# Performance work log

Measured on AMD Instinct MI355X. Metric: run time of the kernel, lower is better.

The kernel has to match this reference:

```python
import jax, jax.numpy as jnp
import numpy as np

D_MODEL = 256; N_LAYERS = 4; INPUT_LEN = 15
D_INNER = 512; D_STATE = 16; D_CONV = 4; DT_RANK = 16
BATCH = 4; SEQ = 2048; EPS = 1e-5

def _ln(x, w, b):
    m = jnp.mean(x, -1, keepdims=True)
    v = jnp.var(x, -1, keepdims=True)
    return (x - m) * jax.lax.rsqrt(v + EPS) * w + b

def _silu(x):
    return x * jax.nn.sigmoid(x)

def _mixer(h, inW, cw, cb, xpW, dtW, dtb, A_log, Dp, opW):
    # h: [B,L,d_model]
    xz = h @ inW.T                      # [B,L,2*D_INNER]
    xh, z = jnp.split(xz, 2, axis=-1)
    # causal depthwise conv1d
    xc = jnp.transpose(xh, (0, 2, 1))   # [B,D,L]
    xc = jax.lax.conv_general_dilated(xc, cw, (1,), [(D_CONV - 1, 0)],
                                      feature_group_count=D_INNER,
                                      dimension_numbers=('NCH', 'OIH', 'NCH'))
    xc = xc + cb[None, :, None]
    xh = _silu(jnp.transpose(xc, (0, 2, 1)))  # [B,L,D]
    dbl = xh @ xpW.T                    # [B,L,DT_RANK+2N]
    dt = dbl[..., :DT_RANK]
    Bm = dbl[..., DT_RANK:DT_RANK + D_STATE]
    C = dbl[..., DT_RANK + D_STATE:]
    dt = jax.nn.softplus(dt @ dtW.T + dtb)    # [B,L,D]
    A = -jnp.exp(A_log)                       # [D,N]
    dA = jnp.exp(dt[..., None] * A)           # [B,L,D,N]
    dBu = dt[..., None] * Bm[:, :, None, :] * xh[..., None]  # [B,L,D,N]
    def step(hst, inp):
        dA_t, dBu_t, C_t = inp
        hst = dA_t * hst + dBu_t
        y = jnp.einsum('bdn,bn->bd', hst, C_t)
        return hst, y
    h0 = jnp.zeros((xh.shape[0], D_INNER, D_STATE), xh.dtype)
    _, ys = jax.lax.scan(step, h0, (jnp.transpose(dA, (1, 0, 2, 3)),
                                    jnp.transpose(dBu, (1, 0, 2, 3)),
                                    jnp.transpose(C, (1, 0, 2))))
    y = jnp.transpose(ys, (1, 0, 2)) + Dp * xh
    y = y * _silu(z)
    return y @ opW.T

def setup_inputs():
    key = jax.random.key(0)
    ks = jax.random.split(key, 8)
    s = 0.02
    return {
        'x_src': jax.random.normal(ks[0], (BATCH, SEQ, INPUT_LEN), jnp.float32),
        'single_eval_pos': 1024,
        'in_W': jax.random.normal(ks[1], (D_MODEL, INPUT_LEN)) * s,
        'norm_w': jnp.ones((N_LAYERS, D_MODEL)),
        'norm_b': jnp.zeros((N_LAYERS, D_MODEL)),
        'inproj_W': jax.random.normal(ks[2], (N_LAYERS, 2 * D_INNER, D_MODEL)) * s,
        'conv_w': jax.random.normal(ks[3], (N_LAYERS, D_INNER, 1, D_CONV)) * 0.2,
        'conv_b': jnp.zeros((N_LAYERS, D_INNER)),
        'xproj_W': jax.random.normal(ks[4], (N_LAYERS, DT_RANK + 2 * D_STATE, D_INNER)) * s,
        'dtproj_W': jax.random.normal(ks[5], (N_LAYERS, D_INNER, DT_RANK)) * 0.1,
        'dtproj_b': jnp.log(jnp.expm1(jnp.full((N_LAYERS, D_INNER), 0.01))),
        'A_log': jnp.log(jnp.broadcast_to(jnp.arange(1, D_STATE + 1, dtype=jnp.float32), (N_LAYERS, D_INNER, D_STATE)) + 0.0),
        'D_param': jnp.ones((N_LAYERS, D_INNER)),
        'outproj_W': jax.random.normal(ks[6], (N_LAYERS, D_MODEL, D_INNER)) * s,
        'out_W': jax.random.normal(ks[7], (1, D_MODEL)) * s,
    }

def reference(x_src, single_eval_pos, in_W, norm_w, norm_b, inproj_W, conv_w, conv_b, xproj_W, dtproj_W, dtproj_b, A_log, D_param, outproj_W, out_W):
    h = x_src @ in_W.T                  # [B,L,d_model]
    res = None
    for i in range(N_LAYERS):
        res = h if res is None else h + res
        hn = _ln(res, norm_w[i], norm_b[i])
        h = _mixer(hn, inproj_W[i], conv_w[i], conv_b[i], xproj_W[i],
                   dtproj_W[i], dtproj_b[i], A_log[i], D_param[i], outproj_W[i])
    # backbone returns hidden_states directly (norm_f defined but not applied)
    return h @ out_W.T                  # [B,L,1]
```

## Files before the change

### kernel.cpp

```cpp
#include <hip/hip_runtime.h>

#define B_   4
#define T_   2048
#define BT_  8192
#define INL  15
#define DM   256
#define DI   512
#define DX   1024
#define DS_  16
#define DR_  16
#define NO_  48
#define NL   4
#define NC_  128
#define LCH  16

typedef short bf16x8 __attribute__((ext_vector_type(8)));
typedef float f32x4  __attribute__((ext_vector_type(4)));

__device__ __forceinline__ float sigmoidf_(float x){
    return __builtin_amdgcn_rcpf(1.f + __expf(-x));
}
__device__ __forceinline__ float softplusf_(float x){
    return fmaxf(x, 0.f) + __logf(1.f + __expf(-fabsf(x)));
}

__device__ __forceinline__ unsigned short f2bf(float x){
    union { float f; unsigned u; } v; v.f = x;
    unsigned r = (v.u + 0x7FFFu + ((v.u >> 16) & 1u)) >> 16;
    return (unsigned short)r;
}
__device__ __forceinline__ float bf2f(unsigned short h){
    union { unsigned u; float f; } v; v.u = ((unsigned)h) << 16;
    return v.f;
}

__device__ __forceinline__ void ld16(const float* __restrict__ p, float* v){
    const float4* q = (const float4*)p;
    float4 x0=q[0],x1=q[1],x2=q[2],x3=q[3];
    v[0]=x0.x; v[1]=x0.y; v[2]=x0.z; v[3]=x0.w;
    v[4]=x1.x; v[5]=x1.y; v[6]=x1.z; v[7]=x1.w;
    v[8]=x2.x; v[9]=x2.y; v[10]=x2.z; v[11]=x2.w;
    v[12]=x3.x; v[13]=x3.y; v[14]=x3.z; v[15]=x3.w;
}
__device__ __forceinline__ void st16(float* __restrict__ p, const float* v){
    float4* q = (float4*)p;
    q[0] = make_float4(v[0],v[1],v[2],v[3]);
    q[1] = make_float4(v[4],v[5],v[6],v[7]);
    q[2] = make_float4(v[8],v[9],v[10],v[11]);
    q[3] = make_float4(v[12],v[13],v[14],v[15]);
}

__global__ void k_cvtW3(const float* __restrict__ W0, unsigned short* __restrict__ h0,
                        unsigned short* __restrict__ l0, int n0,
                        const float* __restrict__ W1, unsigned short* __restrict__ h1,
                        unsigned short* __restrict__ l1, int n1,
                        const float* __restrict__ W2, unsigned short* __restrict__ h2,
                        unsigned short* __restrict__ l2, int n2,
                        const float* __restrict__ opW3, const float* __restrict__ outW,
                        float* __restrict__ cwc){
    int g = blockIdx.x*256 + threadIdx.x;
    const float* W; unsigned short *hi, *lo; int idx;
    if(g < n0){ W = W0; hi = h0; lo = l0; idx = g; }
    else if(g < n0+n1){ W = W1; hi = h1; lo = l1; idx = g - n0; }
    else if(g < n0+n1+n2){ W = W2; hi = h2; lo = l2; idx = g - n0 - n1; }
    else {
        int k = g - (n0+n1+n2);
        if(k < DI){
            float s = 0.f;
#pragma unroll 8
            for(int m=0;m<DM;m++) s += outW[m]*opW3[(size_t)m*DI + k];
            cwc[k] = s;
        }
        return;
    }
    float4 v = ((const float4*)W)[idx];
    ushort4 h, l;
    h.x = f2bf(v.x); l.x = f2bf(v.x - bf2f(h.x));
    h.y = f2bf(v.y); l.y = f2bf(v.y - bf2f(h.y));
    h.z = f2bf(v.z); l.z = f2bf(v.z - bf2f(h.z));
    h.w = f2bf(v.w); l.w = f2bf(v.w - bf2f(h.w));
    ((ushort4*)hi)[idx] = h;
    ((ushort4*)lo)[idx] = l;
}

__global__ void k_inln(const float* __restrict__ x, const float* __restrict__ W,
                       float* __restrict__ res,
                       unsigned short* __restrict__ hnhi, unsigned short* __restrict__ hnlo,
                       const float* __restrict__ w, const float* __restrict__ b){
    int wv = threadIdx.x >> 6, lane = threadIdx.x & 63;
    int bt = blockIdx.x*4 + wv;
    const float* xr = x + bt*INL;
    float xl[INL];
#pragma unroll
    for(int k=0;k<INL;k++) xl[k] = xr[k];
    float4 v;
    float* vv = (float*)&v;
#pragma unroll
    for(int j=0;j<4;j++){
        int m = lane*4 + j;
        const float* wr = W + m*INL;
        float acc = 0.f;
#pragma unroll
        for(int k=0;k<INL;k++) acc += xl[k]*wr[k];
        vv[j] = acc;
    }
    ((float4*)(res + (size_t)bt*DM))[lane] = v;
    float s  = v.x+v.y+v.z+v.w;
    float ss = v.x*v.x+v.y*v.y+v.z*v.z+v.w*v.w;
#pragma unroll
    for(int m=1;m<64;m<<=1){ s += __shfl_xor(s,m); ss += __shfl_xor(ss,m); }
    float mean = s*(1.f/DM);
    float var  = ss*(1.f/DM) - mean*mean;
    float inv  = rsqrtf(var + 1e-5f);
    float4 wt = ((const float4*)w)[lane];
    float4 bs = ((const float4*)b)[lane];
    float4 o;
    o.x = (v.x-mean)*inv*wt.x + bs.x;
    o.y = (v.y-mean)*inv*wt.y + bs.y;
    o.z = (v.z-mean)*inv*wt.z + bs.z;
    o.w = (v.w-mean)*inv*wt.w + bs.w;
    ushort4 hh, ll;
    hh.x = f2bf(o.x); ll.x = f2bf(o.x - bf2f(hh.x));
    hh.y = f2bf(o.y); ll.y = f2bf(o.y - bf2f(hh.y));
    hh.z = f2bf(o.z); ll.z = f2bf(o.z - bf2f(hh.z));
    hh.w = f2bf(o.w); ll.w = f2bf(o.w - bf2f(hh.w));
    ((ushort4*)(hnhi + (size_t)bt*DM))[lane] = hh;
    ((ushort4*)(hnlo + (size_t)bt*DM))[lane] = ll;
}

__global__ void k_resln(const float* __restrict__ res,
                        unsigned short* __restrict__ hnhi, unsigned short* __restrict__ hnlo,
                        const float* __restrict__ w, const float* __restrict__ b){
    int wv = threadIdx.x >> 6, lane = threadIdx.x & 63;
    int bt = blockIdx.x*4 + wv;
    float4 v = ((const float4*)(res + (size_t)bt*DM))[lane];
    float s  = v.x+v.y+v.z+v.w;
    float ss = v.x*v.x+v.y*v.y+v.z*v.z+v.w*v.w;
#pragma unroll
    for(int m=1;m<64;m<<=1){ s += __shfl_xor(s,m); ss += __shfl_xor(ss,m); }
    float mean = s*(1.f/DM);
    float var  = ss*(1.f/DM) - mean*mean;
    float inv  = rsqrtf(var + 1e-5f);
    float4 wt = ((const float4*)w)[lane];
    float4 bs = ((const float4*)b)[lane];
    float4 o;
    o.x = (v.x-mean)*inv*wt.x + bs.x;
    o.y = (v.y-mean)*inv*wt.y + bs.y;
    o.z = (v.z-mean)*inv*wt.z + bs.z;
    o.w = (v.w-mean)*inv*wt.w + bs.w;
    ushort4 hh, ll;
    hh.x = f2bf(o.x); ll.x = f2bf(o.x - bf2f(hh.x));
    hh.y = f2bf(o.y); ll.y = f2bf(o.y - bf2f(hh.y));
    hh.z = f2bf(o.z); ll.z = f2bf(o.z - bf2f(hh.z));
    hh.w = f2bf(o.w); ll.w = f2bf(o.w - bf2f(hh.w));
    ((ushort4*)(hnhi + (size_t)bt*DM))[lane] = hh;
    ((ushort4*)(hnlo + (size_t)bt*DM))[lane] = ll;
}

template<int BM,int BN>
__global__ void __launch_bounds__(256) k_gemm_bf3(
    const unsigned short* __restrict__ Ahi, const unsigned short* __restrict__ Alo,
    const unsigned short* __restrict__ Bhi, const unsigned short* __restrict__ Blo,
    float* __restrict__ C, int M, int N, int K)
{
    constexpr int LDP = 40;
    constexpr int WM = BM/2, WN = BN/2;
    constexpr int MI_ = WM/16, NI_ = WN/16;
    __shared__ unsigned short sAh[BM*LDP], sAl[BM*LDP], sBh[BN*LDP], sBl[BN*LDP];
    int tid  = threadIdx.x;
    int wave = tid >> 6, lane = tid & 63;
    int wm0  = (wave >> 1) * WM, wn0 = (wave & 1) * WN;
    int m0   = blockIdx.y * BM, n0 = blockIdx.x * BN;
    int lr   = lane & 15;
    int kq   = (lane >> 4) * 8;
    int quad4 = (lane >> 4) * 4;

    f32x4 acc[MI_][NI_];
#pragma unroll
    for(int i=0;i<MI_;i++)
#pragma unroll
        for(int j=0;j<NI_;j++) acc[i][j] = (f32x4){0.f,0.f,0.f,0.f};

    for(int k0=0;k0<K;k0+=32){
#pragma unroll
        for(int i=tid;i<BM*4;i+=256){
            int r = i>>2, cg2 = (i&3)*8;
            size_t go = (size_t)(m0+r)*K + k0 + cg2;
            *(float4*)(&sAh[r*LDP + cg2]) = *(const float4*)(Ahi + go);
            *(float4*)(&sAl[r*LDP + cg2]) = *(const float4*)(Alo + go);
        }
#pragma unroll
        for(int i=tid;i<BN*4;i+=256){
            int r = i>>2, cg2 = (i&3)*8;
            size_t go = (size_t)(n0+r)*K + k0 + cg2;
            *(float4*)(&sBh[r*LDP + cg2]) = *(const float4*)(Bhi + go);
            *(float4*)(&sBl[r*LDP + cg2]) = *(const float4*)(Blo + go);
        }
        __syncthreads();
        bf16x8 ah[MI_], al[MI_], bh[NI_], bl[NI_];
#pragma unroll
        for(int mi=0;mi<MI_;mi++){
            int ro = (wm0 + mi*16 + lr)*LDP + kq;
            ah[mi] = *(const bf16x8*)(&sAh[ro]);
            al[mi] = *(const bf16x8*)(&sAl[ro]);
        }
#pragma unroll
        for(int ni=0;ni<NI_;ni++){
            int ro = (wn0 + ni*16 + lr)*LDP + kq;
            bh[ni] = *(const bf16x8*)(&sBh[ro]);
            bl[ni] = *(const bf16x8*)(&sBl[ro]);
        }
#pragma unroll
        for(int mi=0;mi<MI_;mi++)
#pragma unroll
            for(int ni=0;ni<NI_;ni++){
                acc[mi][ni] = __builtin_amdgcn_mfma_f32_16x16x32_bf16(ah[mi], bh[ni], acc[mi][ni], 0,0,0);
                acc[mi][ni] = __builtin_amdgcn_mfma_f32_16x16x32_bf16(ah[mi], bl[ni], acc[mi][ni], 0,0,0);
                acc[mi][ni] = __builtin_amdgcn_mfma_f32_16x16x32_bf16(al[mi], bh[ni], acc[mi][ni], 0,0,0);
            }
        __syncthreads();
    }
#pragma unroll
    for(int mi=0;mi<MI_;mi++)
#pragma unroll
        for(int ni=0;ni<NI_;ni++){
            int col = n0 + wn0 + ni*16 + lr;
#pragma unroll
            for(int r=0;r<4;r++){
                int row = m0 + wm0 + mi*16 + quad4 + r;
                C[(size_t)row*N + col] = acc[mi][ni][r];
            }
        }
}

__global__ void __launch_bounds__(256) k_gemm_pk_res(
    const unsigned* __restrict__ Apk,
    const unsigned short* __restrict__ Bhi, const unsigned short* __restrict__ Blo,
    float* __restrict__ res)
{
    constexpr int BM = 64, BN = 64, K = 512, LDP = 40;
    __shared__ unsigned short sAh[BM*LDP], sAl[BM*LDP], sBh[BN*LDP], sBl[BN*LDP];
    int tid  = threadIdx.x;
    int wave = tid >> 6, lane = tid & 63;
    int wm0  = (wave >> 1) * 32, wn0 = (wave & 1) * 32;
    int m0   = blockIdx.y * BM, n0 = blockIdx.x * BN;
    int lr   = lane & 15;
    int kq   = (lane >> 4) * 8;
    int quad4 = (lane >> 4) * 4;

    f32x4 acc[2][2];
#pragma unroll
    for(int i=0;i<2;i++)
#pragma unroll
        for(int j=0;j<2;j++) acc[i][j] = (f32x4){0.f,0.f,0.f,0.f};

    for(int k0=0;k0<K;k0+=32){
        if(tid < BM*2){
            int r = tid>>1, hf = (tid&1)*16;
            const uint4* yp = (const uint4*)(Apk + (size_t)(m0+r)*K + k0 + hf);
#pragma unroll
            for(int q=0;q<4;q++){
                uint4 p = yp[q];
                ushort4 H, L;
                H.x=(unsigned short)p.x;  L.x=(unsigned short)(p.x>>16);
                H.y=(unsigned short)p.y;  L.y=(unsigned short)(p.y>>16);
                H.z=(unsigned short)p.z;  L.z=(unsigned short)(p.z>>16);
                H.w=(unsigned short)p.w;  L.w=(unsigned short)(p.w>>16);
                *(ushort4*)(&sAh[r*LDP + hf + q*4]) = H;
                *(ushort4*)(&sAl[r*LDP + hf + q*4]) = L;
            }
        }
        {
            int r = tid>>2, cg2 = (tid&3)*8;
            size_t go = (size_t)(n0+r)*K + k0 + cg2;
            *(float4*)(&sBh[r*LDP + cg2]) = *(const float4*)(Bhi + go);
            *(float4*)(&sBl[r*LDP + cg2]) = *(const float4*)(Blo + go);
        }
        __syncthreads();
        bf16x8 ah[2], al[2], bh[2], bl[2];
#pragma unroll
        for(int mi=0;mi<2;mi++){
            int ro = (wm0 + mi*16 + lr)*LDP + kq;
            ah[mi] = *(const bf16x8*)(&sAh[ro]);
            al[mi] = *(const bf16x8*)(&sAl[ro]);
        }
#pragma unroll
        for(int ni=0;ni<2;ni++){
            int ro = (wn0 + ni*16 + lr)*LDP + kq;
            bh[ni] = *(const bf16x8*)(&sBh[ro]);
            bl[ni] = *(const bf16x8*)(&sBl[ro]);
        }
#pragma unroll
        for(int mi=0;mi<2;mi++)
#pragma unroll
            for(int ni=0;ni<2;ni++){
                acc[mi][ni] = __builtin_amdgcn_mfma_f32_16x16x32_bf16(ah[mi], bh[ni], acc[mi][ni], 0,0,0);
                acc[mi][ni] = __builtin_amdgcn_mfma_f32_16x16x32_bf16(ah[mi], bl[ni], acc[mi][ni], 0,0,0);
                acc[mi][ni] = __builtin_amdgcn_mfma_f32_16x16x32_bf16(al[mi], bh[ni], acc[mi][ni], 0,0,0);
            }
        __syncthreads();
    }
#pragma unroll
    for(int mi=0;mi<2;mi++)
#pragma unroll
        for(int ni=0;ni<2;ni++){
            int col = n0 + wn0 + ni*16 + lr;
#pragma unroll
            for(int r=0;r<4;r++){
                int row = m0 + wm0 + mi*16 + quad4 + r;
                size_t o = (size_t)row*DM + col;
                res[o] += acc[mi][ni][r];
            }
        }
}

__global__ void __launch_bounds__(512) k_convxp2(
    const float* __restrict__ xz, const float* __restrict__ cw, const float* __restrict__ cb,
    const unsigned short* __restrict__ Bhi, const unsigned short* __restrict__ Blo,
    const float* __restrict__ dtW, const float* __restrict__ dtbias,
    const float* __restrict__ A_log,
    float* __restrict__ dbl,
    float* __restrict__ S, float* __restrict__ sdt)
{
    __shared__ unsigned short sAh[16*520], sAl[16*520];
    __shared__ float sP[6][16][20];
    __shared__ float sD[16*52];

    int tid = threadIdx.x;
    int wave = tid >> 6, lane = tid & 63;
    int lr = lane & 15, kq = (lane>>4)*8, quad4 = (lane>>4)*4;
    int m0 = blockIdx.x * LCH;
    int d  = tid;
    int nt = wave >> 1, kh = wave & 1;

    float xv[19];
    {
        int rbase = m0 - 3;
        bool mask0 = ((m0 & (T_-1)) == 0);
#pragma unroll
        for(int j=0;j<19;j++)
            xv[j] = (mask0 && j<3) ? 0.f : xz[(size_t)(rbase+j)*DX + d];
    }
    float a_[16]; ld16(A_log + (size_t)d*16, a_);
    float wr_[16]; ld16(dtW + (size_t)d*16, wr_);
    float bsv = dtbias[d];
    float4 w4 = *(const float4*)(cw + d*4);
    float bias = cb[d];
    float vh[16];
#pragma unroll
    for(int t=0;t<16;t++){
        float a = bias + w4.x*xv[t] + w4.y*xv[t+1] + w4.z*xv[t+2] + w4.w*xv[t+3];
        float v = a * sigmoidf_(a);
        vh[t] = v;
        unsigned short hh = f2bf(v);
        sAh[t*520 + d] = hh;
        sAl[t*520 + d] = f2bf(v - bf2f(hh));
    }
    __syncthreads();

    if(wave < 6){
        const unsigned short* bhp = Bhi + (size_t)(nt*16 + lr)*DI + kh*256 + kq;
        const unsigned short* blp = Blo + (size_t)(nt*16 + lr)*DI + kh*256 + kq;
        f32x4 acc = {0.f,0.f,0.f,0.f};
#pragma unroll 4
        for(int ks=0;ks<8;ks++){
            int ao = lr*520 + kh*256 + ks*32 + kq;
            bf16x8 ah = *(const bf16x8*)(&sAh[ao]);
            bf16x8 al = *(const bf16x8*)(&sAl[ao]);
            bf16x8 bh = *(const bf16x8*)(bhp + ks*32);
            bf16x8 bl = *(const bf16x8*)(blp + ks*32);
            acc = __builtin_amdgcn_mfma_f32_16x16x32_bf16(ah, bh, acc, 0,0,0);
            acc = __builtin_amdgcn_mfma_f32_16x16x32_bf16(ah, bl, acc, 0,0,0);
            acc = __builtin_amdgcn_mfma_f32_16x16x32_bf16(al, bh, acc, 0,0,0);
        }
#pragma unroll
        for(int r=0;r<4;r++) sP[wave][quad4+r][lr] = acc[r];
    }
    __syncthreads();

    for(int i=tid;i<768;i+=512){
        int t = i/48, n = i - t*48;
        int nt2 = n >> 4, nn = n & 15;
        float v = sP[nt2*2][t][nn] + sP[nt2*2+1][t][nn];
        dbl[(size_t)(m0+t)*48 + n] = v;
        sD[t*52 + n] = v;
    }
    __syncthreads();

#pragma unroll
    for(int n=0;n<16;n++) a_[n] = -__expf(a_[n]);
    int b = m0 >> 11;
    int c = (m0 & (T_-1)) >> 4;
    float st_[16];
#pragma unroll
    for(int n=0;n<16;n++) st_[n] = 0.f;
    float sd = 0.f;
#pragma unroll 4
    for(int t=0;t<16;t++){
        float dl[16]; ld16(&sD[t*52], dl);
        float bv[16]; ld16(&sD[t*52 + 16], bv);
        float pre = bsv;
#pragma unroll
        for(int r=0;r<16;r++) pre += dl[r]*wr_[r];
        float dtv = softplusf_(pre);
        float dx = dtv*vh[t];
        sd += dtv;
#pragma unroll
        for(int n=0;n<16;n++) st_[n] = __expf(dtv*a_[n])*st_[n] + dx*bv[n];
    }
    st16(S + (((size_t)b*NC_ + c)*DI + d)*16, st_);
    sdt[((size_t)b*NC_ + c)*DI + d] = sd;
}

__global__ void k_scan2(const float* __restrict__ S, const float* __restrict__ sdt,
                        const float* __restrict__ A_log, float* __restrict__ Hinit){
    int g = blockIdx.x*256 + threadIdx.x;
    int b = g >> 13;
    int dn = g & 8191;
    int d = dn >> 4;
    float a = -__expf(A_log[dn]);
    float H = 0.f;
    for(int c0=0;c0<NC_;c0+=8){
        float sv[8], gv[8];
#pragma unroll
        for(int j=0;j<8;j++){
            sv[j] = S[((size_t)(b*NC_ + c0 + j))*8192 + dn];
            gv[j] = sdt[(size_t)(b*NC_ + c0 + j)*DI + d];
        }
#pragma unroll
        for(int j=0;j<8;j++){
            size_t o = ((size_t)(b*NC_ + c0 + j))*8192 + dn;
            Hinit[o] = H;
            H = __expf(gv[j]*a)*H + sv[j];
        }
    }
}

__global__ void __launch_bounds__(256) k_scan3(
    const float* __restrict__ dbl, const float* __restrict__ xz,
    const float* __restrict__ cvw, const float* __restrict__ cvb,
    const float* __restrict__ A_log, const float* __restrict__ Dpar,
    const float* __restrict__ dtW, const float* __restrict__ dtbias,
    const float* __restrict__ Hinit, unsigned* __restrict__ Y)
{
    __shared__ float sbc[16*52];
    int tid = threadIdx.x;
    int c = blockIdx.y, b = blockIdx.z;
    int m0 = b*T_ + c*LCH;
    if(tid < 192){
        int t = tid/12, s = tid - t*12;
        *(float4*)(&sbc[t*52 + s*4]) = *(const float4*)(dbl + (size_t)(m0+t)*48 + s*4);
    }
    __syncthreads();
    int d = blockIdx.x*256 + tid;
    float xv[19];
    {
        int rbase = m0 - 3;
        bool mask0 = (c == 0);
#pragma unroll
        for(int j=0;j<19;j++)
            xv[j] = (mask0 && j<3) ? 0.f : xz[(size_t)(rbase+j)*DX + d];
    }
    float zvp[16];
#pragma unroll
    for(int t=0;t<16;t++) zvp[t] = xz[(size_t)(m0+t)*DX + DI + d];
    float4 w4 = *(const float4*)(cvw + d*4);
    float bias = cvb[d];
    float xhp[16];
#pragma unroll
    for(int t=0;t<16;t++){
        float a = bias + w4.x*xv[t] + w4.y*xv[t+1] + w4.z*xv[t+2] + w4.w*xv[t+3];
        xhp[t] = a * sigmoidf_(a);
    }
    float a_[16]; ld16(A_log + (size_t)d*16, a_);
#pragma unroll
    for(int n=0;n<16;n++) a_[n] = -__expf(a_[n]);
    float wr_[16]; ld16(dtW + (size_t)d*16, wr_);
    float bsv = dtbias[d];
    float st_[16]; ld16(Hinit + (((size_t)b*NC_ + c)*DI + d)*16, st_);
    float Dp = Dpar[d];
#pragma unroll 2
    for(int t=0;t<LCH;t++){
        int bt = m0 + t;
        float dl[16]; ld16(&sbc[t*52], dl);
        float bv[16]; ld16(&sbc[t*52 + 16], bv);
        float cv[16]; ld16(&sbc[t*52 + 32], cv);
        float pre = bsv;
#pragma unroll
        for(int r=0;r<16;r++) pre += dl[r]*wr_[r];
        float dtv = softplusf_(pre);
        float xhv = xhp[t];
        float dx = dtv*xhv;
        float y = 0.f;
#pragma unroll
        for(int n=0;n<16;n++){
            st_[n] = __expf(dtv*a_[n])*st_[n] + dx*bv[n];
            y += st_[n]*cv[n];
        }
        float zv = zvp[t];
        y += Dp*xhv;
        y = y * zv * sigmoidf_(zv);
        unsigned short hh = f2bf(y);
        unsigned short ll = f2bf(y - bf2f(hh));
        Y[(size_t)bt*DI + d] = (unsigned)hh | ((unsigned)ll << 16);
    }
}

__global__ void __launch_bounds__(512) k_scan3o(
    const float* __restrict__ dbl, const float* __restrict__ xz,
    const float* __restrict__ cvw, const float* __restrict__ cvb,
    const float* __restrict__ A_log, const float* __restrict__ Dpar,
    const float* __restrict__ dtW, const float* __restrict__ dtbias,
    const float* __restrict__ Hinit, const float* __restrict__ cwc,
    float* __restrict__ out)
{
    __shared__ float sbc[16*52];
    __shared__ float sW[8][16];
    int tid = threadIdx.x;
    int c = blockIdx.x, b = blockIdx.y;
    int m0 = b*T_ + c*LCH;
    if(tid < 192){
        int t = tid/12, s = tid - t*12;
        *(float4*)(&sbc[t*52 + s*4]) = *(const float4*)(dbl + (size_t)(m0+t)*48 + s*4);
    }
    __syncthreads();
    int d = tid;
    int wave = tid >> 6, lane = tid & 63;
    float xv[19];
    {
        int rbase = m0 - 3;
        bool mask0 = (c == 0);
#pragma unroll
        for(int j=0;j<19;j++)
            xv[j] = (mask0 && j<3) ? 0.f : xz[(size_t)(rbase+j)*DX + d];
    }
    float zvp[16];
#pragma unroll
    for(int t=0;t<16;t++) zvp[t] = xz[(size_t)(m0+t)*DX + DI + d];
    float4 w4 = *(const float4*)(cvw + d*4);
    float bias = cvb[d];
    float xhp[16];
#pragma unroll
    for(int t=0;t<16;t++){
        float a = bias + w4.x*xv[t] + w4.y*xv[t+1] + w4.z*xv[t+2] + w4.w*xv[t+3];
        xhp[t] = a * sigmoidf_(a);
    }
    float a_[16]; ld16(A_log + (size_t)d*16, a_);
#pragma unroll
    for(int n=0;n<16;n++) a_[n] = -__expf(a_[n]);
    float wr_[16]; ld16(dtW + (size_t)d*16, wr_);
    float bsv = dtbias[d];
    float st_[16]; ld16(Hinit + (((size_t)b*NC_ + c)*DI + d)*16, st_);
    float Dp = Dpar[d];
    float cwv = cwc[d];
#pragma unroll 2
    for(int t=0;t<LCH;t++){
        float dl[16]; ld16(&sbc[t*52], dl);
        float bv[16]; ld16(&sbc[t*52 + 16], bv);
        float cv[16]; ld16(&sbc[t*52 + 32], cv);
        float pre = bsv;
#pragma unroll
        for(int r=0;r<16;r++) pre += dl[r]*wr_[r];
        float dtv = softplusf_(pre);
        float xhv = xhp[t];
        float dx = dtv*xhv;
        float y = 0.f;
#pragma unroll
        for(int n=0;n<16;n++){
            st_[n] = __expf(dtv*a_[n])*st_[n] + dx*bv[n];
            y += st_[n]*cv[n];
        }
        float zv = zvp[t];
        y += Dp*xhv;
        y = y * zv * sigmoidf_(zv);
        float s = y * cwv;
#pragma unroll
        for(int m=1;m<64;m<<=1) s += __shfl_xor(s,m);
        if(lane==0) sW[wave][t] = s;
    }
    __syncthreads();
    if(tid < 16){
        float s = 0.f;
#pragma unroll
        for(int w=0;w<8;w++) s += sW[w][tid];
        out[m0 + tid] = s;
    }
}

extern "C" void kernel_launch(void* const* d_in, const int* in_sizes, int n_in,
                              void* d_out, int out_size, void* d_ws, size_t ws_size,
                              hipStream_t stream){
    const float* x_src    = (const float*)d_in[0];
    const float* in_W     = (const float*)d_in[2];
    const float* norm_w   = (const float*)d_in[3];
    const float* norm_b   = (const float*)d_in[4];
    const float* inproj_W = (const float*)d_in[5];
    const float* conv_w   = (const float*)d_in[6];
    const float* conv_b   = (const float*)d_in[7];
    const float* xproj_W  = (const float*)d_in[8];
    const float* dtproj_W = (const float*)d_in[9];
    const float* dtproj_b = (const float*)d_in[10];
    const float* A_log    = (const float*)d_in[11];
    const float* D_param  = (const float*)d_in[12];
    const float* outproj_W= (const float*)d_in[13];
    const float* out_W    = (const float*)d_in[14];

    float* ws  = (float*)d_ws;
    float* res  = ws;
    float* xz   = res  + (size_t)BT_*DM;
    float* dbl  = xz   + (size_t)BT_*DX;
    float* sdtb = dbl  + (size_t)BT_*48;
    float* Sbuf = sdtb + (size_t)B_*NC_*DI;
    float* Hbuf = Sbuf + (size_t)B_*NC_*DI*DS_;
    unsigned short* us = (unsigned short*)(Hbuf + (size_t)B_*NC_*DI*DS_);
    unsigned short* WhiIn  = us;
    unsigned short* WloIn  = WhiIn  + (size_t)NL*DX*DM;
    unsigned short* WhiOut = WloIn  + (size_t)NL*DX*DM;
    unsigned short* WloOut = WhiOut + (size_t)NL*DM*DI;
    unsigned short* WhiXp  = WloOut + (size_t)NL*DM*DI;
    unsigned short* WloXp  = WhiXp  + (size_t)NL*NO_*DI;
    unsigned short* hnhi   = WloXp  + (size_t)NL*NO_*DI;
    unsigned short* hnlo   = hnhi   + (size_t)BT_*DM;
    unsigned*       ybuf   = (unsigned*)(hnlo + (size_t)BT_*DM);
    float*          cwb    = (float*)(ybuf + (size_t)BT_*DI);

    int n0 = NL*DX*DM/4, n1 = NL*DM*DI/4, n2 = NL*NO_*DI/4;
    int nTot = n0 + n1 + n2;
    k_cvtW3<<<(nTot + DI + 255)/256, 256, 0, stream>>>(
        inproj_W,  WhiIn,  WloIn,  n0,
        outproj_W, WhiOut, WloOut, n1,
        xproj_W,   WhiXp,  WloXp,  n2,
        outproj_W + (size_t)3*DM*DI, out_W, cwb);
    k_inln<<<BT_/4, 256, 0, stream>>>(x_src, in_W, res, hnhi, hnlo, norm_w, norm_b);
    for(int i=0;i<NL;i++){
        k_gemm_bf3<128,128><<<dim3(DX/128, BT_/128), 256, 0, stream>>>(
            hnhi, hnlo, WhiIn + (size_t)i*DX*DM, WloIn + (size_t)i*DX*DM, xz, BT_, DX, DM);
        k_convxp2<<<BT_/LCH, 512, 0, stream>>>(xz, conv_w + i*DI*4, conv_b + i*DI,
            WhiXp + (size_t)i*NO_*DI, WloXp + (size_t)i*NO_*DI,
            dtproj_W + (size_t)i*DI*DR_, dtproj_b + i*DI,
            A_log + (size_t)i*DI*DS_, dbl, Sbuf, sdtb);
        k_scan2<<<B_*DI*DS_/256, 256, 0, stream>>>(Sbuf, sdtb, A_log + (size_t)i*DI*DS_, Hbuf);
        if(i < NL-1){
            k_scan3<<<dim3(2, NC_, B_), 256, 0, stream>>>(dbl, xz,
                conv_w + i*DI*4, conv_b + i*DI,
                A_log + (size_t)i*DI*DS_, D_param + i*DI,
                dtproj_W + (size_t)i*DI*DR_, dtproj_b + i*DI, Hbuf, ybuf);
            k_gemm_pk_res<<<dim3(DM/64, BT_/64), 256, 0, stream>>>(
                ybuf, WhiOut + (size_t)i*DM*DI, WloOut + (size_t)i*DM*DI, res);
            k_resln<<<BT_/4, 256, 0, stream>>>(res, hnhi, hnlo,
                norm_w + (i+1)*DM, norm_b + (i+1)*DM);
        } else {
            k_scan3o<<<dim3(NC_, B_), 512, 0, stream>>>(dbl, xz,
                conv_w + i*DI*4, conv_b + i*DI,
                A_log + (size_t)i*DI*DS_, D_param + i*DI,
                dtproj_W + (size_t)i*DI*DR_, dtproj_b + i*DI, Hbuf, cwb,
                (float*)d_out);
        }
    }
}
```

Measured before the change: 549.6 us.

## Merge init kernels, shrink in-proj GEMM tile, halve scan2 block size

Merges the weight-conversion kernel and the input-projection/layernorm kernel into one launch by splitting on block index, removing one kernel launch. Changes the in-projection GEMM tile from 128x128 to 64x128, doubling the number of blocks to fill more CUs. Halves k_scan2 block size to 128 threads so twice as many blocks spread the 32K sequential scans across more CUs. Moves the A_log/dtW/bias loads in k_convxp2 past the MFMA phase to lower register pressure during the conv and projection.

```diff
diff --git a/kernel.cpp b/kernel.cpp
--- a/kernel.cpp
+++ b/kernel.cpp
@@ -14,6 +14,12 @@
 #define NC_  128
 #define LCH  16
 
+#define N0C  (NL*DX*DM/4)
+#define N1C  (NL*DM*DI/4)
+#define N2C  (NL*NO_*DI/4)
+#define NCVT ((N0C + N1C + N2C + DI + 255)/256)
+#define NINL (BT_/4)
+
 typedef short bf16x8 __attribute__((ext_vector_type(8)));
 typedef float f32x4  __attribute__((ext_vector_type(4)));
 
@@ -50,45 +56,47 @@
     q[3] = make_float4(v[12],v[13],v[14],v[15]);
 }
 
-__global__ void k_cvtW3(const float* __restrict__ W0, unsigned short* __restrict__ h0,
-                        unsigned short* __restrict__ l0, int n0,
-                        const float* __restrict__ W1, unsigned short* __restrict__ h1,
-                        unsigned short* __restrict__ l1, int n1,
-                        const float* __restrict__ W2, unsigned short* __restrict__ h2,
-                        unsigned short* __restrict__ l2, int n2,
-                        const float* __restrict__ opW3, const float* __restrict__ outW,
-                        float* __restrict__ cwc){
-    int g = blockIdx.x*256 + threadIdx.x;
-    const float* W; unsigned short *hi, *lo; int idx;
-    if(g < n0){ W = W0; hi = h0; lo = l0; idx = g; }
-    else if(g < n0+n1){ W = W1; hi = h1; lo = l1; idx = g - n0; }
-    else if(g < n0+n1+n2){ W = W2; hi = h2; lo = l2; idx = g - n0 - n1; }
-    else {
-        int k = g - (n0+n1+n2);
-        if(k < DI){
-            float s = 0.f;
-#pragma unroll 8
-            for(int m=0;m<DM;m++) s += outW[m]*opW3[(size_t)m*DI + k];
-            cwc[k] = s;
-        }
-        return;
-    }
-    float4 v = ((const float4*)W)[idx];
-    ushort4 h, l;
-    h.x = f2bf(v.x); l.x = f2bf(v.x - bf2f(h.x));
-    h.y = f2bf(v.y); l.y = f2bf(v.y - bf2f(h.y));
-    h.z = f2bf(v.z); l.z = f2bf(v.z - bf2f(h.z));
-    h.w = f2bf(v.w); l.w = f2bf(v.w - bf2f(h.w));
-    ((ushort4*)hi)[idx] = h;
-    ((ushort4*)lo)[idx] = l;
-}
-
-__global__ void k_inln(const float* __restrict__ x, const float* __restrict__ W,
+__global__ void k_init(const float* __restrict__ W0, unsigned short* __restrict__ h0,
+                       unsigned short* __restrict__ l0,
+                       const float* __restrict__ W1, unsigned short* __restrict__ h1,
+                       unsigned short* __restrict__ l1,
+                       const float* __restrict__ W2, unsigned short* __restrict__ h2,
+                       unsigned short* __restrict__ l2,
+                       const float* __restrict__ opW3, const float* __restrict__ outW,
+                       float* __restrict__ cwc,
+                       const float* __restrict__ x, const float* __restrict__ W,
                        float* __restrict__ res,
                        unsigned short* __restrict__ hnhi, unsigned short* __restrict__ hnlo,
                        const float* __restrict__ w, const float* __restrict__ b){
+    int bid = blockIdx.x;
+    if(bid < NCVT){
+        int g = bid*256 + threadIdx.x;
+        const float* Wp; unsigned short *hi, *lo; int idx;
+        if(g < N0C){ Wp = W0; hi = h0; lo = l0; idx = g; }
+        else if(g < N0C+N1C){ Wp = W1; hi = h1; lo = l1; idx = g - N0C; }
+        else if(g < N0C+N1C+N2C){ Wp = W2; hi = h2; lo = l2; idx = g - N0C - N1C; }
+        else {
+            int k = g - (N0C+N1C+N2C);
+            if(k < DI){
+                float s = 0.f;
+#pragma unroll 8
+                for(int m=0;m<DM;m++) s += outW[m]*opW3[(size_t)m*DI + k];
+                cwc[k] = s;
+            }
+            return;
+        }
+        float4 v = ((const float4*)Wp)[idx];
+        ushort4 h, l;
+        h.x = f2bf(v.x); l.x = f2bf(v.x - bf2f(h.x));
+        h.y = f2bf(v.y); l.y = f2bf(v.y - bf2f(h.y));
+        h.z = f2bf(v.z); l.z = f2bf(v.z - bf2f(h.z));
+        h.w = f2bf(v.w); l.w = f2bf(v.w - bf2f(h.w));
+        ((ushort4*)hi)[idx] = h;
+        ((ushort4*)lo)[idx] = l;
+        return;
+    }
     int wv = threadIdx.x >> 6, lane = threadIdx.x & 63;
-    int bt = blockIdx.x*4 + wv;
+    int bt = (bid - NCVT)*4 + wv;
     const float* xr = x + bt*INL;
     float xl[INL];
 #pragma unroll
@@ -341,9 +349,6 @@
         for(int j=0;j<19;j++)
             xv[j] = (mask0 && j<3) ? 0.f : xz[(size_t)(rbase+j)*DX + d];
     }
-    float a_[16]; ld16(A_log + (size_t)d*16, a_);
-    float wr_[16]; ld16(dtW + (size_t)d*16, wr_);
-    float bsv = dtbias[d];
     float4 w4 = *(const float4*)(cw + d*4);
     float bias = cb[d];
     float vh[16];
@@ -387,8 +392,11 @@
     }
     __syncthreads();
 
+    float a_[16]; ld16(A_log + (size_t)d*16, a_);
 #pragma unroll
     for(int n=0;n<16;n++) a_[n] = -__expf(a_[n]);
+    float wr_[16]; ld16(dtW + (size_t)d*16, wr_);
+    float bsv = dtbias[d];
     int b = m0 >> 11;
     int c = (m0 & (T_-1)) >> 4;
     float st_[16];
@@ -414,7 +422,7 @@
 
 __global__ void k_scan2(const float* __restrict__ S, const float* __restrict__ sdt,
                         const float* __restrict__ A_log, float* __restrict__ Hinit){
-    int g = blockIdx.x*256 + threadIdx.x;
+    int g = blockIdx.x*128 + threadIdx.x;
     int b = g >> 13;
     int dn = g & 8191;
     int d = dn >> 4;
@@ -624,22 +632,20 @@
     unsigned*       ybuf   = (unsigned*)(hnlo + (size_t)BT_*DM);
     float*          cwb    = (float*)(ybuf + (size_t)BT_*DI);
 
-    int n0 = NL*DX*DM/4, n1 = NL*DM*DI/4, n2 = NL*NO_*DI/4;
-    int nTot = n0 + n1 + n2;
-    k_cvtW3<<<(nTot + DI + 255)/256, 256, 0, stream>>>(
-        inproj_W,  WhiIn,  WloIn,  n0,
-        outproj_W, WhiOut, WloOut, n1,
-        xproj_W,   WhiXp,  WloXp,  n2,
-        outproj_W + (size_t)3*DM*DI, out_W, cwb);
-    k_inln<<<BT_/4, 256, 0, stream>>>(x_src, in_W, res, hnhi, hnlo, norm_w, norm_b);
+    k_init<<<NCVT + NINL, 256, 0, stream>>>(
+        inproj_W,  WhiIn,  WloIn,
+        outproj_W, WhiOut, WloOut,
+        xproj_W,   WhiXp,  WloXp,
+        outproj_W + (size_t)3*DM*DI, out_W, cwb,
+        x_src, in_W, res, hnhi, hnlo, norm_w, norm_b);
     for(int i=0;i<NL;i++){
-        k_gemm_bf3<128,128><<<dim3(DX/128, BT_/128), 256, 0, stream>>>(
+        k_gemm_bf3<64,128><<<dim3(DX/128, BT_/64), 256, 0, stream>>>(
             hnhi, hnlo, WhiIn + (size_t)i*DX*DM, WloIn + (size_t)i*DX*DM, xz, BT_, DX, DM);
         k_convxp2<<<BT_/LCH, 512, 0, stream>>>(xz, conv_w + i*DI*4, conv_b + i*DI,
             WhiXp + (size_t)i*NO_*DI, WloXp + (size_t)i*NO_*DI,
             dtproj_W + (size_t)i*DI*DR_, dtproj_b + i*DI,
             A_log + (size_t)i*DI*DS_, dbl, Sbuf, sdtb);
-        k_scan2<<<B_*DI*DS_/256, 256, 0, stream>>>(Sbuf, sdtb, A_log + (size_t)i*DI*DS_, Hbuf);
+        k_scan2<<<B_*DI*DS_/128, 128, 0, stream>>>(Sbuf, sdtb, A_log + (size_t)i*DI*DS_, Hbuf);
         if(i < NL-1){
             k_scan3<<<dim3(2, NC_, B_), 256, 0, stream>>>(dbl, xz,
                 conv_w + i*DI*4, conv_b + i*DI,
```

Result: faster. 529.6 us (median of 3 runs) (-3.6%).
